# Kernel optimization log

Measured on AMD Instinct MI355X. Metric: run time of the kernel, lower is better.

## Reference

```python
import jax, jax.numpy as jnp
import numpy as np
import math

B, S, D, H = 4, 2048, 1024, 16
DH = D // H  # 64
EPS = 1e-5


def setup_inputs() -> dict:
    key = jax.random.key(0)
    ks = jax.random.split(key, 8)
    s = 1.0 / math.sqrt(D)
    return {
        "x": jax.random.normal(ks[0], (B, S, D), dtype=jnp.float32),
        "key_val_lengths": jax.random.randint(ks[1], (B,), 1, S + 1),  # >=1 so no fully-masked row
        "Wq": jax.random.uniform(ks[2], (D, D), jnp.float32, -s, s),
        "bq": jnp.zeros((D,), jnp.float32),
        "Wkv": jax.random.uniform(ks[3], (2 * D, D), jnp.float32, -s, s),
        "bkv": jnp.zeros((2 * D,), jnp.float32),
        "Wo": jax.random.uniform(ks[4], (D, D), jnp.float32, -s, s),
        "bo": jnp.zeros((D,), jnp.float32),
        "ln_g": jnp.ones((D,), jnp.float32),
        "ln_b": jnp.zeros((D,), jnp.float32),
    }


def reference(x, key_val_lengths, Wq, bq, Wkv, bkv, Wo, bo, ln_g, ln_b):
    # Causal self-attention path (query_seq == key_val_seq, is_decoder=True),
    # dropout in eval mode (identity). Faithful to the torch module's math.
    skip = x
    # LayerNorm (applied to both query and key/value since self-attention)
    mu = jnp.mean(x, axis=-1, keepdims=True)
    var = jnp.mean(jnp.square(x - mu), axis=-1, keepdims=True)
    xn = (x - mu) * jax.lax.rsqrt(var + EPS) * ln_g + ln_b

    q = xn @ Wq.T + bq                      # [B,S,D]
    kv = xn @ Wkv.T + bkv                   # [B,S,2D]
    k, v = kv[..., :D], kv[..., D:]

    q = q.reshape(B, S, H, DH)
    k = k.reshape(B, S, H, DH)
    v = v.reshape(B, S, H, DH)

    scores = jnp.einsum("bqhd,bkhd->bhqk", q, k) / math.sqrt(DH)  # [B,H,S,S]

    # padding mask on keys fused with causal mask
    key_pos = jnp.arange(S)
    pad_ok = (key_pos[None, :] < key_val_lengths[:, None])[:, None, None, :]  # [B,1,1,S]
    causal = (key_pos[None, :] <= key_pos[:, None])[None, None, :, :]         # [1,1,S,S]
    scores = jnp.where(pad_ok & causal, scores, -jnp.inf)

    attn = jax.nn.softmax(scores, axis=-1)
    out = jnp.einsum("bhqk,bkhd->bqhd", attn, v).reshape(B, S, D)
    return out @ Wo.T + bo + skip
```

## Files before the change

kernel.cpp:

```cpp
#include <hip/hip_runtime.h>
#include <hip/hip_bf16.h>


#define Bn 4
#define Sn 2048
#define Dn 1024
#define Hn 16
#define DHn 64
#define Mn (Bn*Sn)

typedef short short8 __attribute__((ext_vector_type(8)));
typedef short short4v __attribute__((ext_vector_type(4)));
typedef unsigned short ushort8 __attribute__((ext_vector_type(8)));
typedef unsigned short ushort4v __attribute__((ext_vector_type(4)));
typedef float f32x4 __attribute__((ext_vector_type(4)));

__device__ inline float bf2f(unsigned short u) {
    union { unsigned int i; float f; } c;
    c.i = ((unsigned int)u) << 16;
    return c.f;
}

__device__ inline unsigned short f2bf(float f) {
    union { float f; unsigned int i; } c;
    c.f = f;
    unsigned int i = c.i;
    unsigned int lsb = (i >> 16) & 1;
    i += 0x7fffu + lsb;
    return (unsigned short)(i >> 16);
}

__device__ inline unsigned short f2bf_t(float f) {
    union { float f; unsigned int i; } c;
    c.f = f;
    return (unsigned short)(c.i >> 16);
}

__device__ __forceinline__ float fast_exp2(float x) {
#if __has_builtin(__builtin_amdgcn_exp2f)
    return __builtin_amdgcn_exp2f(x);
#else
    return exp2f(x);
#endif
}

#if __has_builtin(__builtin_amdgcn_global_load_lds)
#define HAVE_GLDS 1
__device__ __forceinline__ void glds16(const void* g, void* l) {
    __builtin_amdgcn_global_load_lds(
        (const __attribute__((address_space(1))) unsigned int*)g,
        (__attribute__((address_space(3))) unsigned int*)l, 16, 0, 0);
}
#else
#define HAVE_GLDS 0
#endif

__global__ __launch_bounds__(256) void f2bf3_kernel(const float* __restrict__ Wq,
                                                    const float* __restrict__ Wkv,
                                                    const float* __restrict__ Wo,
                                                    unsigned short* __restrict__ oq,
                                                    unsigned short* __restrict__ okv,
                                                    unsigned short* __restrict__ oo) {
    int i = blockIdx.x * 256 + threadIdx.x;
    const float* src;
    unsigned short* dst;
    int off;
    if (i < 262144) { src = Wq; dst = oq; off = i; }
    else if (i < 786432) { src = Wkv; dst = okv; off = i - 262144; }
    else { src = Wo; dst = oo; off = i - 786432; }
    float4 v = *(const float4*)(src + (size_t)off * 4);
    ushort4v r;
    r.x = f2bf(v.x); r.y = f2bf(v.y); r.z = f2bf(v.z); r.w = f2bf(v.w);
    *(ushort4v*)(dst + (size_t)off * 4) = r;
}

__global__ __launch_bounds__(256) void ln_kernel(const float* __restrict__ x,
                                                 const float* __restrict__ g,
                                                 const float* __restrict__ bta,
                                                 unsigned short* __restrict__ xn) {
    int row = blockIdx.x;
    int t = threadIdx.x;
    const float* xr = x + (size_t)row * Dn;
    float4 v = *(const float4*)(xr + t * 4);
    float s = v.x + v.y + v.z + v.w;
    float sq = v.x * v.x + v.y * v.y + v.z * v.z + v.w * v.w;
    for (int off = 32; off; off >>= 1) {
        s += __shfl_down(s, off);
        sq += __shfl_down(sq, off);
    }
    __shared__ float ss[4], ssq[4];
    int wave = t >> 6, lane = t & 63;
    if (lane == 0) { ss[wave] = s; ssq[wave] = sq; }
    __syncthreads();
    float tot = ss[0] + ss[1] + ss[2] + ss[3];
    float totq = ssq[0] + ssq[1] + ssq[2] + ssq[3];
    float mean = tot * (1.0f / Dn);
    float var = totq * (1.0f / Dn) - mean * mean;
    float rstd = rsqrtf(var + 1e-5f);
    float4 gv = *(const float4*)(g + t * 4);
    float4 bv = *(const float4*)(bta + t * 4);
    ushort4v r;
    r.x = f2bf((v.x - mean) * rstd * gv.x + bv.x);
    r.y = f2bf((v.y - mean) * rstd * gv.y + bv.y);
    r.z = f2bf((v.z - mean) * rstd * gv.z + bv.z);
    r.w = f2bf((v.w - mean) * rstd * gv.w + bv.w);
    *(ushort4v*)(xn + (size_t)row * Dn + t * 4) = r;
}

template <bool ADD_SKIP, bool OUT_BF16>
__global__ __launch_bounds__(256, 2) void gemm_bt(const unsigned short* __restrict__ A,
                                                  const unsigned short* __restrict__ Bw,
                                                  const float* __restrict__ bias,
                                                  const float* __restrict__ skip,
                                                  void* __restrict__ Cout,
                                                  int M, int N, int K) {
    __shared__ unsigned short As[128 * 32];
    __shared__ unsigned short Bs[128 * 32];
    const int tid = threadIdx.x;
    const int wave = tid >> 6, lane = tid & 63;
    const int warp_m = wave & 1, warp_n = wave >> 1;
    const int bm = blockIdx.x, bn = blockIdx.y;
    const int l4 = lane & 3, lr = lane >> 2;
    const int quad = lane >> 4, r16 = lane & 15;

    f32x4 acc[4][4];
#pragma unroll
    for (int i = 0; i < 4; i++)
#pragma unroll
        for (int j = 0; j < 4; j++) acc[i][j] = (f32x4){0.f, 0.f, 0.f, 0.f};

    for (int k0 = 0; k0 < K; k0 += 32) {
        __syncthreads();
#if HAVE_GLDS
#pragma unroll
        for (int i = 0; i < 2; ++i) {
            int inst = wave + 4 * i;
            glds16(A + (size_t)(bm * 128 + inst * 16 + lr) * K + k0 + l4 * 8, &As[inst * 512]);
            glds16(Bw + (size_t)(bn * 128 + inst * 16 + lr) * K + k0 + l4 * 8, &Bs[inst * 512]);
        }
#else
#pragma unroll
        for (int i = 0; i < 2; ++i) {
            int inst = wave + 4 * i;
            int row = inst * 16 + lr;
            ushort8 a = *(const ushort8*)(A + (size_t)(bm * 128 + row) * K + k0 + l4 * 8);
            ushort8 b2 = *(const ushort8*)(Bw + (size_t)(bn * 128 + row) * K + k0 + l4 * 8);
            *(ushort8*)(As + inst * 512 + lane * 8) = a;
            *(ushort8*)(Bs + inst * 512 + lane * 8) = b2;
        }
#endif
        __syncthreads();

        short8 afr[4], bfr[4];
#pragma unroll
        for (int i = 0; i < 4; ++i) {
            int row = warp_m * 64 + i * 16 + r16;
            afr[i] = *(const short8*)(As + row * 32 + quad * 8);
        }
#pragma unroll
        for (int j = 0; j < 4; ++j) {
            int row = warp_n * 64 + j * 16 + r16;
            bfr[j] = *(const short8*)(Bs + row * 32 + quad * 8);
        }
#pragma unroll
        for (int i = 0; i < 4; ++i)
#pragma unroll
            for (int j = 0; j < 4; ++j)
                acc[i][j] = __builtin_amdgcn_mfma_f32_16x16x32_bf16(afr[i], bfr[j], acc[i][j], 0, 0, 0);
    }

#pragma unroll
    for (int j = 0; j < 4; ++j) {
        int gcol = bn * 128 + warp_n * 64 + j * 16 + r16;
        float bv = bias[gcol];
#pragma unroll
        for (int i = 0; i < 4; ++i) {
#pragma unroll
            for (int r = 0; r < 4; ++r) {
                int grow = bm * 128 + warp_m * 64 + i * 16 + quad * 4 + r;
                float v = acc[i][j][r] + bv;
                size_t idx = (size_t)grow * N + gcol;
                if (ADD_SKIP) v += skip[idx];
                if (OUT_BF16)
                    ((unsigned short*)Cout)[idx] = f2bf(v);
                else
                    ((float*)Cout)[idx] = v;
            }
        }
    }
}

#define STK 72
#define STV 68
#define STP 72

__global__ __launch_bounds__(256, 4) void attn_kernel(const unsigned short* __restrict__ Q,
                                                      const unsigned short* __restrict__ KV,
                                                      const int* __restrict__ lens,
                                                      unsigned short* __restrict__ Ctx) {
    const int qt = blockIdx.x, h = blockIdx.y, b = blockIdx.z;
    const int tid = threadIdx.x;
    const int wave = tid >> 6, lane = tid & 63;
    const int quad = lane >> 4, c = lane & 15;
    const int len = lens[b];
    const int qw = qt * 64 + wave * 16;
    const int myq = qw + c;

    __shared__ unsigned short Ks[64 * STK];
    __shared__ unsigned short Vt[64 * STV];
    __shared__ unsigned short Ps[4][16 * STP];

    short8 qfrag[2];
    {
        const unsigned short* qp2 = Q + ((size_t)(b * Sn + qw + c)) * Dn + h * 64 + quad * 8;
        qfrag[0] = *(const short8*)(qp2);
        qfrag[1] = *(const short8*)(qp2 + 32);
    }

    f32x4 acc_o[4];
#pragma unroll
    for (int j = 0; j < 4; j++) acc_o[j] = (f32x4){0.f, 0.f, 0.f, 0.f};
    float m_run = -1e30f, l_run = 0.f;

    const int krow = tid >> 2, dp = tid & 3;
    const int kg = tid >> 4, dg = tid & 15;
    const unsigned short* kvb = KV + ((size_t)(b * Sn)) * (2 * Dn) + h * 64;

    ushort8 kr0, kr1;
    ushort4v vr0, vr1, vr2, vr3;
    {
        const unsigned short* kp2 = kvb + (size_t)krow * (2 * Dn) + dp * 16;
        kr0 = *(const ushort8*)(kp2);
        kr1 = *(const ushort8*)(kp2 + 8);
        const unsigned short* vp2 = kvb + Dn + (size_t)(kg * 4) * (2 * Dn) + dg * 4;
        vr0 = *(const ushort4v*)(vp2);
        vr1 = *(const ushort4v*)(vp2 + 2 * Dn);
        vr2 = *(const ushort4v*)(vp2 + 4 * Dn);
        vr3 = *(const ushort4v*)(vp2 + 6 * Dn);
    }

    const float C2 = 0.18033688011112042f;
    const int ktend = min(qt, (len - 1) >> 6);
    for (int kt = 0; kt <= ktend; ++kt) {
        __syncthreads();
        *(ushort8*)(&Ks[krow * STK + dp * 16]) = kr0;
        *(ushort8*)(&Ks[krow * STK + dp * 16 + 8]) = kr1;
#pragma unroll
        for (int w = 0; w < 4; ++w) {
            ushort4v t;
            t.x = vr0[w]; t.y = vr1[w]; t.z = vr2[w]; t.w = vr3[w];
            *(ushort4v*)(&Vt[(dg * 4 + w) * STV + kg * 4]) = t;
        }
        __syncthreads();

        if (kt < ktend) {
            const unsigned short* kp2 = kvb + (size_t)((kt + 1) * 64 + krow) * (2 * Dn) + dp * 16;
            kr0 = *(const ushort8*)(kp2);
            kr1 = *(const ushort8*)(kp2 + 8);
            const unsigned short* vp2 = kvb + Dn + (size_t)((kt + 1) * 64 + kg * 4) * (2 * Dn) + dg * 4;
            vr0 = *(const ushort4v*)(vp2);
            vr1 = *(const ushort4v*)(vp2 + 2 * Dn);
            vr2 = *(const ushort4v*)(vp2 + 4 * Dn);
            vr3 = *(const ushort4v*)(vp2 + 6 * Dn);
        }

        f32x4 sacc[4];
#pragma unroll
        for (int mt = 0; mt < 4; ++mt) sacc[mt] = (f32x4){0.f, 0.f, 0.f, 0.f};
#pragma unroll
        for (int mt = 0; mt < 4; ++mt) {
            short8 kf0 = *(const short8*)(&Ks[(mt * 16 + c) * STK + quad * 8]);
            short8 kf1 = *(const short8*)(&Ks[(mt * 16 + c) * STK + 32 + quad * 8]);
            sacc[mt] = __builtin_amdgcn_mfma_f32_16x16x32_bf16(kf0, qfrag[0], sacc[mt], 0, 0, 0);
            sacc[mt] = __builtin_amdgcn_mfma_f32_16x16x32_bf16(kf1, qfrag[1], sacc[mt], 0, 0, 0);
        }

        const int kb = kt * 64;
        const bool full = (kb + 63 <= qw) && (kb + 64 <= len);
        float sv[16];
        float mx = -1e30f;
        if (full) {
#pragma unroll
            for (int e = 0; e < 16; ++e) {
                float v = sacc[e >> 2][e & 3];
                sv[e] = v;
                mx = fmaxf(mx, v);
            }
        } else {
#pragma unroll
            for (int mt = 0; mt < 4; ++mt) {
#pragma unroll
                for (int r = 0; r < 4; ++r) {
                    int kpos = kb + mt * 16 + quad * 4 + r;
                    bool valid = (kpos <= myq) && (kpos < len);
                    float v = valid ? sacc[mt][r] : -1e30f;
                    sv[mt * 4 + r] = v;
                    mx = fmaxf(mx, v);
                }
            }
        }
        mx = fmaxf(mx, __shfl_xor(mx, 16));
        mx = fmaxf(mx, __shfl_xor(mx, 32));
        float mnew = fmaxf(m_run, mx * C2);
        float alpha = fast_exp2(m_run - mnew);
        m_run = mnew;
        l_run *= alpha;

        float ar_[4];
#pragma unroll
        for (int r = 0; r < 4; ++r) ar_[r] = __shfl(alpha, quad * 4 + r);
#pragma unroll
        for (int j = 0; j < 4; ++j)
#pragma unroll
            for (int r = 0; r < 4; ++r) acc_o[j][r] *= ar_[r];

#pragma unroll
        for (int mt = 0; mt < 4; ++mt) {
            float p0 = fast_exp2(__builtin_fmaf(sv[mt * 4 + 0], C2, -mnew));
            float p1 = fast_exp2(__builtin_fmaf(sv[mt * 4 + 1], C2, -mnew));
            float p2 = fast_exp2(__builtin_fmaf(sv[mt * 4 + 2], C2, -mnew));
            float p3 = fast_exp2(__builtin_fmaf(sv[mt * 4 + 3], C2, -mnew));
            l_run += (p0 + p1) + (p2 + p3);
            ushort4v pw;
            pw.x = f2bf_t(p0); pw.y = f2bf_t(p1); pw.z = f2bf_t(p2); pw.w = f2bf_t(p3);
            *(ushort4v*)(&Ps[wave][c * STP + mt * 16 + quad * 4]) = pw;
        }

#pragma unroll
        for (int ks = 0; ks < 2; ++ks) {
            short8 pf = *(const short8*)(&Ps[wave][c * STP + ks * 32 + quad * 8]);
#pragma unroll
            for (int j = 0; j < 4; ++j) {
                const unsigned short* vb2 = &Vt[(j * 16 + c) * STV + ks * 32 + quad * 8];
                short4v a0 = *(const short4v*)(vb2);
                short4v a1 = *(const short4v*)(vb2 + 4);
                short8 vf = __builtin_shufflevector(a0, a1, 0, 1, 2, 3, 4, 5, 6, 7);
                acc_o[j] = __builtin_amdgcn_mfma_f32_16x16x32_bf16(pf, vf, acc_o[j], 0, 0, 0);
            }
        }
    }

    l_run += __shfl_xor(l_run, 16);
    l_run += __shfl_xor(l_run, 32);
    float li[4];
#pragma unroll
    for (int r = 0; r < 4; ++r) {
        float lv = __shfl(l_run, quad * 4 + r);
        li[r] = 1.0f / lv;
    }
#pragma unroll
    for (int r = 0; r < 4; ++r) {
        unsigned short* cp = Ctx + ((size_t)(b * Sn + qw + quad * 4 + r)) * Dn + h * 64 + c;
#pragma unroll
        for (int j = 0; j < 4; ++j) {
            cp[j * 16] = f2bf(acc_o[j][r] * li[r]);
        }
    }
}

extern "C" void kernel_launch(void* const* d_in, const int* in_sizes, int n_in,
                              void* d_out, int out_size, void* d_ws, size_t ws_size,
                              hipStream_t stream) {
    const float* x = (const float*)d_in[0];
    const int* lens = (const int*)d_in[1];
    const float* Wq = (const float*)d_in[2];
    const float* bq = (const float*)d_in[3];
    const float* Wkv = (const float*)d_in[4];
    const float* bkv = (const float*)d_in[5];
    const float* Wo = (const float*)d_in[6];
    const float* bo = (const float*)d_in[7];
    const float* ln_g = (const float*)d_in[8];
    const float* ln_b = (const float*)d_in[9];
    float* out = (float*)d_out;

    char* ws = (char*)d_ws;
    unsigned short* xn_bf = (unsigned short*)ws;
    unsigned short* wq_bf = (unsigned short*)(ws + (size_t)16 * 1024 * 1024);
    unsigned short* wkv_bf = (unsigned short*)(ws + (size_t)18 * 1024 * 1024);
    unsigned short* wo_bf = (unsigned short*)(ws + (size_t)22 * 1024 * 1024);
    unsigned short* q_bf = (unsigned short*)(ws + (size_t)24 * 1024 * 1024);
    unsigned short* kv_bf = (unsigned short*)(ws + (size_t)40 * 1024 * 1024);
    unsigned short* ctx_bf = (unsigned short*)(ws + (size_t)72 * 1024 * 1024);

    f2bf3_kernel<<<4096, 256, 0, stream>>>(Wq, Wkv, Wo, wq_bf, wkv_bf, wo_bf);

    ln_kernel<<<Mn, 256, 0, stream>>>(x, ln_g, ln_b, xn_bf);

    {
        dim3 grid(Mn / 128, Dn / 128);
        gemm_bt<false, true><<<grid, 256, 0, stream>>>(xn_bf, wq_bf, bq, nullptr,
                                                       (void*)q_bf, Mn, Dn, Dn);
    }
    {
        dim3 grid(Mn / 128, 2 * Dn / 128);
        gemm_bt<false, true><<<grid, 256, 0, stream>>>(xn_bf, wkv_bf, bkv, nullptr,
                                                       (void*)kv_bf, Mn, 2 * Dn, Dn);
    }
    {
        dim3 grid(Sn / 64, Hn, Bn);
        attn_kernel<<<grid, 256, 0, stream>>>(q_bf, kv_bf, lens, ctx_bf);
    }
    {
        dim3 grid(Mn / 128, Dn / 128);
        gemm_bt<true, false><<<grid, 256, 0, stream>>>(ctx_bf, wo_bf, bo, x,
                                                       (void*)out, Mn, Dn, Dn);
    }
}
```

Before: 288.9 us.

## Fuse Q and KV projections and pair causal query tiles in attention

Merges the Q and KV projection GEMMs into one GEMM writing an interleaved QKV buffer, with per-column-block bias selection. The attention kernel now processes two query tiles per block, one early and one late, so causal work is balanced across blocks and each K/V tile load serves both tiles. This removes a kernel launch and the causal tail imbalance, at the cost of doubled accumulator and register state per thread, which may pressure occupancy.

```diff
diff --git a/kernel.cpp b/kernel.cpp
--- a/kernel.cpp
+++ b/kernel.cpp
@@ -111,6 +111,8 @@
 __global__ __launch_bounds__(256, 2) void gemm_bt(const unsigned short* __restrict__ A,
                                                   const unsigned short* __restrict__ Bw,
                                                   const float* __restrict__ bias,
+                                                  const float* __restrict__ bias2,
+                                                  int bsplit,
                                                   const float* __restrict__ skip,
                                                   void* __restrict__ Cout,
                                                   int M, int N, int K) {
@@ -169,10 +171,11 @@
                 acc[i][j] = __builtin_amdgcn_mfma_f32_16x16x32_bf16(afr[i], bfr[j], acc[i][j], 0, 0, 0);
     }
 
+    const float* bp = (bn * 128 >= bsplit) ? (bias2 - bsplit) : bias;
 #pragma unroll
     for (int j = 0; j < 4; ++j) {
         int gcol = bn * 128 + warp_n * 64 + j * 16 + r16;
-        float bv = bias[gcol];
+        float bv = bp[gcol];
 #pragma unroll
         for (int i = 0; i < 4; ++i) {
 #pragma unroll
@@ -193,77 +196,69 @@
 #define STK 72
 #define STV 68
 #define STP 72
-
-__global__ __launch_bounds__(256, 4) void attn_kernel(const unsigned short* __restrict__ Q,
-                                                      const unsigned short* __restrict__ KV,
+#define QKVS (3 * Dn)
+
+__global__ __launch_bounds__(256, 4) void attn_kernel(const unsigned short* __restrict__ QKV,
                                                       const int* __restrict__ lens,
                                                       unsigned short* __restrict__ Ctx) {
-    const int qt = blockIdx.x, h = blockIdx.y, b = blockIdx.z;
+    const int h = blockIdx.y, b = blockIdx.z;
+    const int qtA = blockIdx.x;
+    const int qtB = (Sn / 64 - 1) - qtA;
     const int tid = threadIdx.x;
     const int wave = tid >> 6, lane = tid & 63;
     const int quad = lane >> 4, c = lane & 15;
     const int len = lens[b];
-    const int qw = qt * 64 + wave * 16;
-    const int myq = qw + c;
+    const int lt = (len - 1) >> 6;
+    const int ktendA = min(qtA, lt);
+    const int ktendB = min(qtB, lt);
+    const int qwA = qtA * 64 + wave * 16;
+    const int qwB = qtB * 64 + wave * 16;
+    const int myqA = qwA + c, myqB = qwB + c;
 
     __shared__ unsigned short Ks[64 * STK];
     __shared__ unsigned short Vt[64 * STV];
     __shared__ unsigned short Ps[4][16 * STP];
 
-    short8 qfrag[2];
+    short8 qfA[2], qfB[2];
     {
-        const unsigned short* qp2 = Q + ((size_t)(b * Sn + qw + c)) * Dn + h * 64 + quad * 8;
-        qfrag[0] = *(const short8*)(qp2);
-        qfrag[1] = *(const short8*)(qp2 + 32);
-    }
-
-    f32x4 acc_o[4];
-#pragma unroll
-    for (int j = 0; j < 4; j++) acc_o[j] = (f32x4){0.f, 0.f, 0.f, 0.f};
-    float m_run = -1e30f, l_run = 0.f;
+        const unsigned short* qa = QKV + (size_t)(b * Sn + qwA + c) * QKVS + h * 64 + quad * 8;
+        qfA[0] = *(const short8*)(qa);
+        qfA[1] = *(const short8*)(qa + 32);
+        const unsigned short* qb = QKV + (size_t)(b * Sn + qwB + c) * QKVS + h * 64 + quad * 8;
+        qfB[0] = *(const short8*)(qb);
+        qfB[1] = *(const short8*)(qb + 32);
+    }
+
+    f32x4 accA[4], accB[4];
+#pragma unroll
+    for (int j = 0; j < 4; j++) {
+        accA[j] = (f32x4){0.f, 0.f, 0.f, 0.f};
+        accB[j] = (f32x4){0.f, 0.f, 0.f, 0.f};
+    }
+    float mA = -1e30f, lA = 0.f, mB = -1e30f, lB = 0.f;
 
     const int krow = tid >> 2, dp = tid & 3;
     const int kg = tid >> 4, dg = tid & 15;
-    const unsigned short* kvb = KV + ((size_t)(b * Sn)) * (2 * Dn) + h * 64;
+    const unsigned short* kbase = QKV + (size_t)(b * Sn) * QKVS + Dn + h * 64;
+    const unsigned short* vbase = QKV + (size_t)(b * Sn) * QKVS + 2 * Dn + h * 64;
 
     ushort8 kr0, kr1;
     ushort4v vr0, vr1, vr2, vr3;
     {
-        const unsigned short* kp2 = kvb + (size_t)krow * (2 * Dn) + dp * 16;
+        const unsigned short* kp2 = kbase + (size_t)krow * QKVS + dp * 16;
         kr0 = *(const ushort8*)(kp2);
         kr1 = *(const ushort8*)(kp2 + 8);
-        const unsigned short* vp2 = kvb + Dn + (size_t)(kg * 4) * (2 * Dn) + dg * 4;
+        const unsigned short* vp2 = vbase + (size_t)(kg * 4) * QKVS + dg * 4;
         vr0 = *(const ushort4v*)(vp2);
-        vr1 = *(const ushort4v*)(vp2 + 2 * Dn);
-        vr2 = *(const ushort4v*)(vp2 + 4 * Dn);
-        vr3 = *(const ushort4v*)(vp2 + 6 * Dn);
+        vr1 = *(const ushort4v*)(vp2 + QKVS);
+        vr2 = *(const ushort4v*)(vp2 + 2 * QKVS);
+        vr3 = *(const ushort4v*)(vp2 + 3 * QKVS);
     }
 
     const float C2 = 0.18033688011112042f;
-    const int ktend = min(qt, (len - 1) >> 6);
-    for (int kt = 0; kt <= ktend; ++kt) {
-        __syncthreads();
-        *(ushort8*)(&Ks[krow * STK + dp * 16]) = kr0;
-        *(ushort8*)(&Ks[krow * STK + dp * 16 + 8]) = kr1;
-#pragma unroll
-        for (int w = 0; w < 4; ++w) {
-            ushort4v t;
-            t.x = vr0[w]; t.y = vr1[w]; t.z = vr2[w]; t.w = vr3[w];
-            *(ushort4v*)(&Vt[(dg * 4 + w) * STV + kg * 4]) = t;
-        }
-        __syncthreads();
-
-        if (kt < ktend) {
-            const unsigned short* kp2 = kvb + (size_t)((kt + 1) * 64 + krow) * (2 * Dn) + dp * 16;
-            kr0 = *(const ushort8*)(kp2);
-            kr1 = *(const ushort8*)(kp2 + 8);
-            const unsigned short* vp2 = kvb + Dn + (size_t)((kt + 1) * 64 + kg * 4) * (2 * Dn) + dg * 4;
-            vr0 = *(const ushort4v*)(vp2);
-            vr1 = *(const ushort4v*)(vp2 + 2 * Dn);
-            vr2 = *(const ushort4v*)(vp2 + 4 * Dn);
-            vr3 = *(const ushort4v*)(vp2 + 6 * Dn);
-        }
-
+
+    auto process = [&](int kt, const short8* qf, f32x4* acc_o, float& m_run, float& l_run,
+                       int qw, int myq) {
         f32x4 sacc[4];
 #pragma unroll
         for (int mt = 0; mt < 4; ++mt) sacc[mt] = (f32x4){0.f, 0.f, 0.f, 0.f};
@@ -271,8 +266,8 @@
         for (int mt = 0; mt < 4; ++mt) {
             short8 kf0 = *(const short8*)(&Ks[(mt * 16 + c) * STK + quad * 8]);
             short8 kf1 = *(const short8*)(&Ks[(mt * 16 + c) * STK + 32 + quad * 8]);
-            sacc[mt] = __builtin_amdgcn_mfma_f32_16x16x32_bf16(kf0, qfrag[0], sacc[mt], 0, 0, 0);
-            sacc[mt] = __builtin_amdgcn_mfma_f32_16x16x32_bf16(kf1, qfrag[1], sacc[mt], 0, 0, 0);
+            sacc[mt] = __builtin_amdgcn_mfma_f32_16x16x32_bf16(kf0, qf[0], sacc[mt], 0, 0, 0);
+            sacc[mt] = __builtin_amdgcn_mfma_f32_16x16x32_bf16(kf1, qf[1], sacc[mt], 0, 0, 0);
         }
 
         const int kb = kt * 64;
@@ -338,24 +333,56 @@
                 acc_o[j] = __builtin_amdgcn_mfma_f32_16x16x32_bf16(pf, vf, acc_o[j], 0, 0, 0);
             }
         }
-    }
-
-    l_run += __shfl_xor(l_run, 16);
-    l_run += __shfl_xor(l_run, 32);
-    float li[4];
-#pragma unroll
-    for (int r = 0; r < 4; ++r) {
-        float lv = __shfl(l_run, quad * 4 + r);
-        li[r] = 1.0f / lv;
-    }
-#pragma unroll
-    for (int r = 0; r < 4; ++r) {
-        unsigned short* cp = Ctx + ((size_t)(b * Sn + qw + quad * 4 + r)) * Dn + h * 64 + c;
-#pragma unroll
-        for (int j = 0; j < 4; ++j) {
-            cp[j * 16] = f2bf(acc_o[j][r] * li[r]);
-        }
-    }
+    };
+
+    for (int kt = 0; kt <= ktendB; ++kt) {
+        __syncthreads();
+        *(ushort8*)(&Ks[krow * STK + dp * 16]) = kr0;
+        *(ushort8*)(&Ks[krow * STK + dp * 16 + 8]) = kr1;
+#pragma unroll
+        for (int w = 0; w < 4; ++w) {
+            ushort4v t;
+            t.x = vr0[w]; t.y = vr1[w]; t.z = vr2[w]; t.w = vr3[w];
+            *(ushort4v*)(&Vt[(dg * 4 + w) * STV + kg * 4]) = t;
+        }
+        __syncthreads();
+
+        if (kt < ktendB) {
+            const unsigned short* kp2 = kbase + (size_t)((kt + 1) * 64 + krow) * QKVS + dp * 16;
+            kr0 = *(const ushort8*)(kp2);
+            kr1 = *(const ushort8*)(kp2 + 8);
+            const unsigned short* vp2 = vbase + (size_t)((kt + 1) * 64 + kg * 4) * QKVS + dg * 4;
+            vr0 = *(const ushort4v*)(vp2);
+            vr1 = *(const ushort4v*)(vp2 + QKVS);
+            vr2 = *(const ushort4v*)(vp2 + 2 * QKVS);
+            vr3 = *(const ushort4v*)(vp2 + 3 * QKVS);
+        }
+
+        if (kt <= ktendA)
+            process(kt, qfA, accA, mA, lA, qwA, myqA);
+        process(kt, qfB, accB, mB, lB, qwB, myqB);
+    }
+
+    auto finalize = [&](f32x4* acc_o, float l_run, int qw) {
+        l_run += __shfl_xor(l_run, 16);
+        l_run += __shfl_xor(l_run, 32);
+        float li[4];
+#pragma unroll
+        for (int r = 0; r < 4; ++r) {
+            float lv = __shfl(l_run, quad * 4 + r);
+            li[r] = 1.0f / lv;
+        }
+#pragma unroll
+        for (int r = 0; r < 4; ++r) {
+            unsigned short* cp = Ctx + ((size_t)(b * Sn + qw + quad * 4 + r)) * Dn + h * 64 + c;
+#pragma unroll
+            for (int j = 0; j < 4; ++j) {
+                cp[j * 16] = f2bf(acc_o[j][r] * li[r]);
+            }
+        }
+    };
+    finalize(accA, lA, qwA);
+    finalize(accB, lB, qwB);
 }
 
 extern "C" void kernel_launch(void* const* d_in, const int* in_sizes, int n_in,
@@ -378,31 +405,25 @@
     unsigned short* wq_bf = (unsigned short*)(ws + (size_t)16 * 1024 * 1024);
     unsigned short* wkv_bf = (unsigned short*)(ws + (size_t)18 * 1024 * 1024);
     unsigned short* wo_bf = (unsigned short*)(ws + (size_t)22 * 1024 * 1024);
-    unsigned short* q_bf = (unsigned short*)(ws + (size_t)24 * 1024 * 1024);
-    unsigned short* kv_bf = (unsigned short*)(ws + (size_t)40 * 1024 * 1024);
+    unsigned short* qkv_bf = (unsigned short*)(ws + (size_t)24 * 1024 * 1024);
     unsigned short* ctx_bf = (unsigned short*)(ws + (size_t)72 * 1024 * 1024);
 
     f2bf3_kernel<<<4096, 256, 0, stream>>>(Wq, Wkv, Wo, wq_bf, wkv_bf, wo_bf);
 
     ln_kernel<<<Mn, 256, 0, stream>>>(x, ln_g, ln_b, xn_bf);
 
+    {
+        dim3 grid(Mn / 128, 3 * Dn / 128);
+        gemm_bt<false, true><<<grid, 256, 0, stream>>>(xn_bf, wq_bf, bq, bkv, Dn, nullptr,
+                                                       (void*)qkv_bf, Mn, 3 * Dn, Dn);
+    }
+    {
+        dim3 grid(Sn / 128, Hn, Bn);
+        attn_kernel<<<grid, 256, 0, stream>>>(qkv_bf, lens, ctx_bf);
+    }
     {
         dim3 grid(Mn / 128, Dn / 128);
-        gemm_bt<false, true><<<grid, 256, 0, stream>>>(xn_bf, wq_bf, bq, nullptr,
-                                                       (void*)q_bf, Mn, Dn, Dn);
-    }
-    {
-        dim3 grid(Mn / 128, 2 * Dn / 128);
-        gemm_bt<false, true><<<grid, 256, 0, stream>>>(xn_bf, wkv_bf, bkv, nullptr,
-                                                       (void*)kv_bf, Mn, 2 * Dn, Dn);
-    }
-    {
-        dim3 grid(Sn / 64, Hn, Bn);
-        attn_kernel<<<grid, 256, 0, stream>>>(q_bf, kv_bf, lens, ctx_bf);
-    }
-    {
-        dim3 grid(Mn / 128, Dn / 128);
-        gemm_bt<true, false><<<grid, 256, 0, stream>>>(ctx_bf, wo_bf, bo, x,
+        gemm_bt<true, false><<<grid, 256, 0, stream>>>(ctx_bf, wo_bf, bo, bo, Dn, x,
                                                        (void*)out, Mn, Dn, Dn);
     }
 }
```

Result: faster. 270.2 us (-6.5%).
